# Kernel tuning notes

Measured on AMD Instinct MI355X. Metric: run time of the kernel, lower is better.

Reference implementation:

```python
import jax, jax.numpy as jnp
import numpy as np

S, B, I = 512, 32, 512
H, O = 512, 512
TOP_K = 5
TRUNC = 100
EPS = 1e-7
NEG = -1e9


def setup_inputs() -> dict:
    key = jax.random.key(0)
    ks = jax.random.split(key, 12)
    std = 1.0 / np.sqrt(H)
    return {
        "input": jax.random.normal(ks[0], (S, B, I), jnp.float32),
        "h0": jax.random.normal(ks[1], (1, B, H), jnp.float32),
        "c0": jax.random.normal(ks[2], (1, B, H), jnp.float32),
        "mem0": jax.random.normal(ks[3], (1, B, H), jnp.float32),
        # LSTMCell params (PyTorch layout: gates ordered i, f, g, o)
        "w_ih": jax.random.uniform(ks[4], (4 * H, I), jnp.float32, -std, std),
        "w_hh": jax.random.uniform(ks[5], (4 * H, H), jnp.float32, -std, std),
        "b_ih": jax.random.uniform(ks[6], (4 * H,), jnp.float32, -std, std),
        "b_hh": jax.random.uniform(ks[7], (4 * H,), jnp.float32, -std, std),
        # attention scorer, init N(0, 0.01)
        "w_t": jax.random.normal(ks[8], (2 * H, 1), jnp.float32) * 0.01,
        "fc_w": jax.random.uniform(ks[9], (O, 2 * H), jnp.float32, -1.0 / np.sqrt(2 * H), 1.0 / np.sqrt(2 * H)),
        "fc_b": jax.random.uniform(ks[10], (O,), jnp.float32, -1.0 / np.sqrt(2 * H), 1.0 / np.sqrt(2 * H)),
    }


def _sab_forward(input, h0, c0, mem0, w_ih, w_hh, b_ih, b_hh, w_t, fc_w, fc_b):
    seq_len, batch, _ = input.shape
    hid = w_hh.shape[1]
    m0 = mem0.shape[0]
    mmax = m0 + seq_len  # remem_every_k == 1: one append per step
    mem_buf = jnp.zeros((mmax, batch, hid), input.dtype).at[:m0].set(mem0)
    pos = jnp.arange(mmax)

    def step(carry, xs):
        h, c, mem = carry
        x, i = xs
        trunc = ((i + 1) % TRUNC) == 0
        h_in = jnp.where(trunc, jax.lax.stop_gradient(h), h)
        c_in = jnp.where(trunc, jax.lax.stop_gradient(c), c)
        # LSTM cell
        gates = x @ w_ih.T + b_ih + h_in @ w_hh.T + b_hh
        gi, gf, gg, go = jnp.split(gates, 4, axis=1)
        c_new = jax.nn.sigmoid(gf) * c_in + jax.nn.sigmoid(gi) * jnp.tanh(gg)
        h_new = jax.nn.sigmoid(go) * jnp.tanh(c_new)
        # attention over current (valid) memory
        cur = m0 + i  # valid memory entries before appending
        valid = (pos < cur)[:, None]  # (mmax, 1)
        feat = jnp.tanh(jnp.concatenate([jnp.broadcast_to(h_new[None], (mmax, batch, hid)), mem], axis=2))
        scores = jnp.einsum("mbf,fo->mb", feat, w_t)  # (mmax, batch)
        s_mask = jnp.where(valid, scores, NEG)
        kth = jax.lax.top_k(s_mask.T, TOP_K)[0][:, -1]  # (batch,)
        min_valid = jnp.min(jnp.where(valid, scores, jnp.inf), axis=0)
        delta = jnp.where(cur <= TOP_K, min_valid, kth) + EPS
        aw = jnp.clip(s_mask - delta[None, :], 0.0)  # invalid rows -> 0
        aw = aw / (jnp.sum(aw, axis=0, keepdims=True) + EPS)
        m_t = jnp.einsum("mb,mbh->bh", aw, mem)
        h_out = h_new + m_t
        mem = jax.lax.dynamic_update_slice(mem, h_out[None], (cur, 0, 0))
        return (h_out, c_new, mem), (h_out, m_t)

    (h_f, c_f, mem_f), (h_seq, m_seq) = jax.lax.scan(
        step, (h0[0], c0[0], mem_buf), (input, jnp.arange(seq_len)))
    out = jnp.concatenate([h_seq, m_seq], axis=2) @ fc_w.T + fc_b  # (S,B,O)
    return out, h_f[None], c_f[None], mem_f


def reference(input, h0, c0, mem0, w_ih, w_hh, b_ih, b_hh, w_t, fc_w, fc_b):
    return _sab_forward(input, h0, c0, mem0, w_ih, w_hh, b_ih, b_hh, w_t, fc_w, fc_b)
```

## Files before the change

kernel.cpp:

```cpp
#include <hip/hip_runtime.h>

#define SEQ   512
#define NB    32
#define NH    512
#define BH    16384
#define EPSF  1e-7f
#define NWG   64

#define HF_OFF  8388608
#define CF_OFF  8404992
#define MEM_OFF 8421376

#define X0_OFF   0ul
#define X1_OFF   16777216ul
#define WI0_OFF  33554432ul
#define WI1_OFF  35651584ul
#define HH_OFF   37748736ul
#define HMF_OFF  54558720ul
#define MSEQ_OFF 71368704ul
#define FCW_OFF  88145920ul
#define S2P_OFF  89194496ul
#define BAR_OFF  93396992ul
#define GX_OFF   93405184ul

typedef __attribute__((ext_vector_type(8))) short bf16x8;
typedef __attribute__((ext_vector_type(4))) float f32x4;
typedef __attribute__((ext_vector_type(4))) int   i32x4;

__device__ __forceinline__ unsigned short f2bf(float f){
  unsigned u = __float_as_uint(f);
  unsigned r = (u + 0x7fffu + ((u >> 16) & 1u)) >> 16;
  return (unsigned short)r;
}
__device__ __forceinline__ float bf2f(unsigned short h){
  return __uint_as_float(((unsigned)h) << 16);
}
__device__ __forceinline__ float sigmf(float x){ return 1.f/(1.f + __expf(-x)); }
__device__ __forceinline__ float tanhff(float x){
  x = fminf(20.f, fmaxf(-20.f, x));
  float e = __expf(-2.f*x);
  return (1.f - e)/(1.f + e);
}

__device__ __forceinline__ void store16_cc(void* p, i32x4 v){
  asm volatile("global_store_dwordx4 %0, %1, off sc0 sc1" :: "v"(p), "v"(v) : "memory");
}

__global__ void phase0(const float* __restrict__ x, const float* __restrict__ h0,
                       const float* __restrict__ mem0, const float* __restrict__ fcw,
                       const float* __restrict__ wih,
                       unsigned short* __restrict__ x0, unsigned short* __restrict__ x1,
                       unsigned short* __restrict__ wi0, unsigned short* __restrict__ wi1,
                       unsigned short* __restrict__ hh, unsigned short* __restrict__ hmf,
                       unsigned short* __restrict__ fcwb,
                       float* __restrict__ mem_row0, unsigned* __restrict__ bar){
  long i = (long)blockIdx.x * blockDim.x + threadIdx.x;
  if (i < (long)SEQ*BH){
    float v = x[i];
    unsigned short a = f2bf(v);
    x0[i]=a; x1[i]=f2bf(v - bf2f(a));
  }
  if (i < 2048*512){
    float v = wih[i];
    unsigned short a = f2bf(v);
    wi0[i]=a; wi1[i]=f2bf(v - bf2f(a));
  }
  if (i < 512*1024) fcwb[i] = f2bf(fcw[i]);
  if (i < BH){
    float h = h0[i];
    unsigned short a = f2bf(h);
    int b = (int)(i >> 9), col = (int)(i & 511);
    long d = (long)(col>>3)*256 + b*8 + (col&7);
    hh[d]=a; hmf[d]=f2bf(h - bf2f(a));
    mem_row0[i] = mem0[i];
  }
  if (i < 2048) bar[i] = 0u;
}

__launch_bounds__(256)
__global__ void xgemm(const unsigned short* __restrict__ x0, const unsigned short* __restrict__ x1,
                      const unsigned short* __restrict__ wi0, const unsigned short* __restrict__ wi1,
                      const float* __restrict__ bih, const float* __restrict__ bhh,
                      float* __restrict__ gx){
  const int tid = threadIdx.x;
  const int wave = tid >> 6, lane = tid & 63, quad = lane >> 4, ln = lane & 15;
  const int rowb = blockIdx.x*64 + wave*16;
  const int colb = blockIdx.y*64;
  const long aoff = (long)(rowb + ln)*512 + quad*8;
  f32x4 acc[4] = {{0,0,0,0},{0,0,0,0},{0,0,0,0},{0,0,0,0}};
  #pragma unroll 4
  for (int ki = 0; ki < 16; ++ki){
    bf16x8 a0 = *(const bf16x8*)(x0 + aoff + ki*32);
    bf16x8 a1 = *(const bf16x8*)(x1 + aoff + ki*32);
    #pragma unroll
    for (int n = 0; n < 4; ++n){
      long bo = (long)(colb + n*16 + ln)*512 + quad*8 + ki*32;
      bf16x8 b0 = *(const bf16x8*)(wi0 + bo);
      bf16x8 b1 = *(const bf16x8*)(wi1 + bo);
      acc[n] = __builtin_amdgcn_mfma_f32_16x16x32_bf16(a0, b0, acc[n], 0,0,0);
      acc[n] = __builtin_amdgcn_mfma_f32_16x16x32_bf16(a0, b1, acc[n], 0,0,0);
      acc[n] = __builtin_amdgcn_mfma_f32_16x16x32_bf16(a1, b0, acc[n], 0,0,0);
    }
  }
  #pragma unroll
  for (int n = 0; n < 4; ++n){
    int col = colb + n*16 + ln;
    float bias = bih[col] + bhh[col];
    #pragma unroll
    for (int rr = 0; rr < 4; ++rr){
      int row = rowb + quad*4 + rr;
      gx[(long)row*2048 + col] = acc[n][rr] + bias;
    }
  }
}

__launch_bounds__(256, 1)
__global__ void recurrent(unsigned short* __restrict__ hh,
                          unsigned short* __restrict__ hmf,
                          unsigned short* __restrict__ mseq,
                          float* __restrict__ s2p,
                          unsigned* __restrict__ bar,
                          float* __restrict__ dout,
                          const float* __restrict__ gx,
                          const float* __restrict__ whh,
                          const float* __restrict__ wt,
                          const float* __restrict__ c0){
  const int g    = blockIdx.x;
  const int tid  = threadIdx.x;
  const int wave = tid >> 6, lane = tid & 63, quad = lane >> 4, ln = lane & 15;
  const int mtile = wave & 1, ntile = wave >> 1;

  __shared__ float gates_lds[32*33];
  __shared__ float s2v[64*33];
  __shared__ float wt_lds[32*5];
  __shared__ int   repl_lds[32];
  __shared__ unsigned hm_lds[256];
  __shared__ float s2_lds[32];

  bf16x8 fW0[16], fW1[16];
  {
    int cl   = ntile*16 + ln;
    int gate = cl >> 3, jl = cl & 7;
    long grow = (long)(gate*NH + g*8 + jl);
    const float* wh = whh + grow*NH;
    #pragma unroll
    for (int ki = 0; ki < 16; ++ki){
      int k0 = ki*32 + quad*8;
      bf16x8 a, b;
      #pragma unroll
      for (int e = 0; e < 8; ++e){
        float vh = wh[k0+e];
        unsigned short w0 = f2bf(vh);
        a[e] = (short)w0; b[e] = (short)f2bf(vh - bf2f(w0));
      }
      fW0[ki]=a; fW1[ki]=b;
    }
  }

  const int b_  = tid >> 3, jl_ = tid & 7;
  const int jg_ = g*8 + jl_;
  const float wt2 = wt[NH + jg_];
  float creg = c0[b_*NH + jg_];
  float* memf = dout + MEM_OFF;

  float m0v = memf[b_*NH + jg_];
  float va0 = 0.f, va1 = 0.f, va2 = 0.f, va3 = 0.f, va4 = 0.f;
  float hoprev = m0v;

  {
    float v = tanhff(m0v) * wt2;
    v += __shfl_xor(v, 1); v += __shfl_xor(v, 2); v += __shfl_xor(v, 4);
    if (jl_ == 0)
      __hip_atomic_store((unsigned*)(s2p + g*32 + b_), __float_as_uint(v),
                         __ATOMIC_RELAXED, __HIP_MEMORY_SCOPE_AGENT);
  }

  const float* gxr0 = gx + (long)b_*2048 + jg_;
  float gxi = gxr0[0], gxf = gxr0[512], gxg = gxr0[1024], gxo = gxr0[1536];

  float tv0=-3e38f,tv1=-3e38f,tv2=-3e38f,tv3=-3e38f,tv4=-3e38f;

  unsigned epoch = 1u;
  __syncthreads();
  if (tid == 0)
    __hip_atomic_store(&bar[g*32], epoch, __ATOMIC_RELAXED, __HIP_MEMORY_SCOPE_AGENT);
  if (tid < 64){
    while (true){
      unsigned v = __hip_atomic_load(&bar[tid*32], __ATOMIC_RELAXED, __HIP_MEMORY_SCOPE_AGENT);
      if (__all((int)(v >= epoch))) break;
    }
  }
  __syncthreads();

  const int arow = mtile*16 + ln;

  #pragma unroll 1
  for (int t = 0; t < SEQ; ++t){
    f32x4 sv0, sv1, sv2, sv3, sv4, sv5, sv6, sv7;
    if (tid < 64){
      const float* sp = s2p + (long)t*2048 + tid*32;
      sv0 = *(const f32x4*)(sp +  0); sv1 = *(const f32x4*)(sp +  4);
      sv2 = *(const f32x4*)(sp +  8); sv3 = *(const f32x4*)(sp + 12);
      sv4 = *(const f32x4*)(sp + 16); sv5 = *(const f32x4*)(sp + 20);
      sv6 = *(const f32x4*)(sp + 24); sv7 = *(const f32x4*)(sp + 28);
    }

    const unsigned short* p0 = hh  + (long)t*BH + quad*256 + arow*8;
    const unsigned short* p1 = hmf + (long)t*BH + quad*256 + arow*8;
    f32x4 acc0 = {0.f,0.f,0.f,0.f}, acc1 = {0.f,0.f,0.f,0.f};
    #pragma unroll
    for (int ki = 0; ki < 16; ++ki){
      bf16x8 aH = *(const bf16x8*)(p0 + ki*1024);
      bf16x8 aM = *(const bf16x8*)(p1 + ki*1024);
      acc0 = __builtin_amdgcn_mfma_f32_16x16x32_bf16(aH, fW0[ki], acc0, 0,0,0);
      acc1 = __builtin_amdgcn_mfma_f32_16x16x32_bf16(aH, fW1[ki], acc1, 0,0,0);
      if (ki & 1) acc1 = __builtin_amdgcn_mfma_f32_16x16x32_bf16(aM, fW0[ki], acc1, 0,0,0);
      else        acc0 = __builtin_amdgcn_mfma_f32_16x16x32_bf16(aM, fW0[ki], acc0, 0,0,0);
    }
    #pragma unroll
    for (int r = 0; r < 4; ++r){
      int brow = mtile*16 + quad*4 + r;
      gates_lds[brow*33 + ntile*16 + ln] = acc0[r] + acc1[r];
    }

    if (tid < 64){
      float* sr = &s2v[tid*33];
      *(f32x4*)(sr +  0) = sv0; *(f32x4*)(sr +  4) = sv1;
      *(f32x4*)(sr +  8) = sv2; *(f32x4*)(sr + 12) = sv3;
      *(f32x4*)(sr + 16) = sv4; *(f32x4*)(sr + 20) = sv5;
      *(f32x4*)(sr + 24) = sv6; *(f32x4*)(sr + 28) = sv7;
    }
    if (tid < 32){
      float s0=0.f,s1=0.f,s2s=0.f,s3=0.f;
      #pragma unroll
      for (int q = 0; q < 64; q += 4){
        s0  += s2v[(q  )*33 + tid];
        s1  += s2v[(q+1)*33 + tid];
        s2s += s2v[(q+2)*33 + tid];
        s3  += s2v[(q+3)*33 + tid];
      }
      float s = (s0+s1) + (s2s+s3);
      int repl = -1;
      if (t < 5){
        repl = t;
        if      (t==0) tv0=s;
        else if (t==1) tv1=s;
        else if (t==2) tv2=s;
        else if (t==3) tv3=s;
        else           tv4=s;
      } else {
        float mn = fminf(fminf(fminf(tv0,tv1),fminf(tv2,tv3)),tv4);
        if (s > mn){
          if      (tv0==mn){tv0=s;repl=0;}
          else if (tv1==mn){tv1=s;repl=1;}
          else if (tv2==mn){tv2=s;repl=2;}
          else if (tv3==mn){tv3=s;repl=3;}
          else             {tv4=s;repl=4;}
        }
      }
      int cnt = (t+1 < 5) ? (t+1) : 5;
      float mn = tv0;
      if (cnt>1) mn = fminf(mn, tv1);
      if (cnt>2) mn = fminf(mn, tv2);
      if (cnt>3) mn = fminf(mn, tv3);
      if (cnt>4) mn = fminf(mn, tv4);
      float thr = mn + EPSF;
      float w0 =            fmaxf(tv0-thr,0.f);
      float w1 = (cnt>1) ? fmaxf(tv1-thr,0.f) : 0.f;
      float w2 = (cnt>2) ? fmaxf(tv2-thr,0.f) : 0.f;
      float w3 = (cnt>3) ? fmaxf(tv3-thr,0.f) : 0.f;
      float w4 = (cnt>4) ? fmaxf(tv4-thr,0.f) : 0.f;
      float inv = 1.f/((w0+w1+w2+w3+w4) + EPSF);
      wt_lds[tid*5+0]=w0*inv;
      wt_lds[tid*5+1]=w1*inv;
      wt_lds[tid*5+2]=w2*inv;
      wt_lds[tid*5+3]=w3*inv;
      wt_lds[tid*5+4]=w4*inv;
      repl_lds[tid]=repl;
    }
    __syncthreads();

    float g0 = gates_lds[b_*33 + jl_     ] + gxi;
    float g1 = gates_lds[b_*33 +  8 + jl_] + gxf;
    float g2 = gates_lds[b_*33 + 16 + jl_] + gxg;
    float g3 = gates_lds[b_*33 + 24 + jl_] + gxo;
    float ig = sigmf(g0), fg = sigmf(g1), gg = tanhff(g2), og = sigmf(g3);
    creg = fg*creg + ig*gg;
    float hn = og * tanhff(creg);

    int rp = repl_lds[b_];
    va0 = (rp==0) ? hoprev : va0;
    va1 = (rp==1) ? hoprev : va1;
    va2 = (rp==2) ? hoprev : va2;
    va3 = (rp==3) ? hoprev : va3;
    va4 = (rp==4) ? hoprev : va4;
    float mt = wt_lds[b_*5+0]*va0 + wt_lds[b_*5+1]*va1 + wt_lds[b_*5+2]*va2
             + wt_lds[b_*5+3]*va3 + wt_lds[b_*5+4]*va4;
    float ho = hn + mt;
    long eoff = (long)b_*NH + jg_;
    memf[(long)(t+1)*BH + eoff] = ho;
    unsigned short h0s = f2bf(ho);
    unsigned short h1s = f2bf(ho - bf2f(h0s));
    hm_lds[b_*8 + jl_] = (unsigned)h0s | (((unsigned)h1s) << 16);
    mseq[(long)t*BH + eoff] = f2bf(mt);
    if (t == SEQ-1) dout[HF_OFF + eoff] = ho;
    hoprev = ho;

    {
      float v = tanhff(ho) * wt2;
      v += __shfl_xor(v, 1); v += __shfl_xor(v, 2); v += __shfl_xor(v, 4);
      if (jl_ == 0) s2_lds[b_] = v;
    }

    {
      int tn = (t+1 < SEQ) ? t+1 : t;
      const float* gxr = gx + ((long)tn*32 + b_)*2048 + jg_;
      gxi = gxr[0]; gxf = gxr[512]; gxg = gxr[1024]; gxo = gxr[1536];
    }

    __syncthreads();
    ++epoch;
    if (tid < 64){
      if (tid < 32){
        int b = tid;
        unsigned q0 = hm_lds[b*8+0], q1 = hm_lds[b*8+1], q2 = hm_lds[b*8+2], q3 = hm_lds[b*8+3];
        unsigned q4 = hm_lds[b*8+4], q5 = hm_lds[b*8+5], q6 = hm_lds[b*8+6], q7 = hm_lds[b*8+7];
        i32x4 hi, mi;
        hi[0] = (int)((q0 & 0xffffu) | (q1 << 16));
        hi[1] = (int)((q2 & 0xffffu) | (q3 << 16));
        hi[2] = (int)((q4 & 0xffffu) | (q5 << 16));
        hi[3] = (int)((q6 & 0xffffu) | (q7 << 16));
        mi[0] = (int)((q0 >> 16) | (q1 & 0xffff0000u));
        mi[1] = (int)((q2 >> 16) | (q3 & 0xffff0000u));
        mi[2] = (int)((q4 >> 16) | (q5 & 0xffff0000u));
        mi[3] = (int)((q6 >> 16) | (q7 & 0xffff0000u));
        long d = (long)(t+1)*BH + g*256 + b*8;
        store16_cc(hh  + d, hi);
        store16_cc(hmf + d, mi);
      } else if (tid < 40){
        int q = tid - 32;
        f32x4 svp = *(const f32x4*)&s2_lds[q*4];
        store16_cc(s2p + (long)(t+1)*2048 + g*32 + q*4, __builtin_bit_cast(i32x4, svp));
      }
      asm volatile("s_waitcnt vmcnt(0)" ::: "memory");
      if (tid == 0)
        __hip_atomic_store(&bar[g*32], epoch, __ATOMIC_RELAXED, __HIP_MEMORY_SCOPE_AGENT);
      while (true){
        unsigned v = __hip_atomic_load(&bar[tid*32], __ATOMIC_RELAXED, __HIP_MEMORY_SCOPE_AGENT);
        if (__all((int)(v >= epoch))) break;
      }
    }
    __syncthreads();
  }
  dout[CF_OFF + (long)b_*NH + jg_] = creg;
}

__launch_bounds__(256)
__global__ void outgemm(const unsigned short* __restrict__ hh,
                        const unsigned short* __restrict__ mseq,
                        const unsigned short* __restrict__ fcwb,
                        const float* __restrict__ fcb,
                        float* __restrict__ out){
  const int tid = threadIdx.x;
  const int wave = tid >> 6, lane = tid & 63, quad = lane >> 4, ln = lane & 15;
  const int wgM = blockIdx.x;
  const int wgN = blockIdx.y;
  const int r = wgM*64 + wave*16 + ln;
  const int s = r >> 5, b = r & 31;
  const unsigned short* pa_h = hh   + (long)(s+1)*BH + quad*256 + b*8;
  const unsigned short* pa_m = mseq + (long)s*BH     + (long)b*NH + quad*8;
  const unsigned short* pb   = fcwb + (long)(wgN*64 + ln)*1024 + quad*8;
  f32x4 accs[4] = {{0,0,0,0},{0,0,0,0},{0,0,0,0},{0,0,0,0}};
  #pragma unroll 4
  for (int ki = 0; ki < 16; ++ki){
    bf16x8 a = *(const bf16x8*)(pa_h + ki*1024);
    #pragma unroll
    for (int n = 0; n < 4; ++n){
      bf16x8 bb = *(const bf16x8*)(pb + (long)n*16*1024 + ki*32);
      accs[n] = __builtin_amdgcn_mfma_f32_16x16x32_bf16(a, bb, accs[n], 0,0,0);
    }
  }
  #pragma unroll 4
  for (int ki = 0; ki < 16; ++ki){
    bf16x8 a = *(const bf16x8*)(pa_m + ki*32);
    #pragma unroll
    for (int n = 0; n < 4; ++n){
      bf16x8 bb = *(const bf16x8*)(pb + 512 + (long)n*16*1024 + ki*32);
      accs[n] = __builtin_amdgcn_mfma_f32_16x16x32_bf16(a, bb, accs[n], 0,0,0);
    }
  }
  #pragma unroll
  for (int n = 0; n < 4; ++n){
    int o = wgN*64 + n*16 + ln;
    float bias = fcb[o];
    #pragma unroll
    for (int rr = 0; rr < 4; ++rr){
      int row = wgM*64 + wave*16 + quad*4 + rr;
      out[(long)row*512 + o] = accs[n][rr] + bias;
    }
  }
}

extern "C" void kernel_launch(void* const* d_in, const int* in_sizes, int n_in,
                              void* d_out, int out_size, void* d_ws, size_t ws_size,
                              hipStream_t stream){
  (void)in_sizes; (void)n_in; (void)out_size; (void)ws_size;
  const float* x    = (const float*)d_in[0];
  const float* h0   = (const float*)d_in[1];
  const float* c0   = (const float*)d_in[2];
  const float* mem0 = (const float*)d_in[3];
  const float* wih  = (const float*)d_in[4];
  const float* whh  = (const float*)d_in[5];
  const float* bih  = (const float*)d_in[6];
  const float* bhh  = (const float*)d_in[7];
  const float* wt   = (const float*)d_in[8];
  const float* fcw  = (const float*)d_in[9];
  const float* fcb  = (const float*)d_in[10];
  float* out = (float*)d_out;
  char* ws = (char*)d_ws;

  unsigned short* x0   = (unsigned short*)(ws + X0_OFF);
  unsigned short* x1   = (unsigned short*)(ws + X1_OFF);
  unsigned short* wi0  = (unsigned short*)(ws + WI0_OFF);
  unsigned short* wi1  = (unsigned short*)(ws + WI1_OFF);
  unsigned short* hh   = (unsigned short*)(ws + HH_OFF);
  unsigned short* hmf  = (unsigned short*)(ws + HMF_OFF);
  unsigned short* mseq = (unsigned short*)(ws + MSEQ_OFF);
  unsigned short* fcwb = (unsigned short*)(ws + FCW_OFF);
  float*          s2p  = (float*)(ws + S2P_OFF);
  unsigned*       bar  = (unsigned*)(ws + BAR_OFF);
  float*          gx   = (float*)(ws + GX_OFF);

  phase0<<<32768, 256, 0, stream>>>(x, h0, mem0, fcw, wih,
                                    x0, x1, wi0, wi1,
                                    hh, hmf, fcwb, out + MEM_OFF, bar);
  xgemm<<<dim3(256, 32), 256, 0, stream>>>(x0, x1, wi0, wi1, bih, bhh, gx);
  recurrent<<<NWG, 256, 0, stream>>>(hh, hmf, mseq, s2p, bar, out,
                                     gx, whh, wt, c0);
  outgemm<<<dim3(256, 8), 256, 0, stream>>>(hh, mseq, fcwb, fcb, out);
}
```

Before: 4.561 ms.

## Add a fifth wave to compute attention scores concurrently with the gate MFMA

The recurrent kernel grows from 256 to 320 threads. The extra wave reads the per-step score partials directly from global memory, reduces them and runs the top-k and weight update, while the four original waves run the hidden-state MFMA at the same time. This removes the LDS staging buffer for the scores and takes that reduction off the critical path of the MFMA waves. In exchange, the extra wave makes strided global loads, and the block gets more threads, which can lengthen barrier costs.

```diff
diff --git a/kernel.cpp b/kernel.cpp
--- a/kernel.cpp
+++ b/kernel.cpp
@@ -114,7 +114,7 @@
   }
 }
 
-__launch_bounds__(256, 1)
+__launch_bounds__(320, 1)
 __global__ void recurrent(unsigned short* __restrict__ hh,
                           unsigned short* __restrict__ hmf,
                           unsigned short* __restrict__ mseq,
@@ -131,14 +131,13 @@
   const int mtile = wave & 1, ntile = wave >> 1;
 
   __shared__ float gates_lds[32*33];
-  __shared__ float s2v[64*33];
   __shared__ float wt_lds[32*5];
   __shared__ int   repl_lds[32];
   __shared__ unsigned hm_lds[256];
   __shared__ float s2_lds[32];
 
   bf16x8 fW0[16], fW1[16];
-  {
+  if (wave < 4){
     int cl   = ntile*16 + ln;
     int gate = cl >> 3, jl = cl & 7;
     long grow = (long)(gate*NH + g*8 + jl);
@@ -160,14 +159,16 @@
   const int b_  = tid >> 3, jl_ = tid & 7;
   const int jg_ = g*8 + jl_;
   const float wt2 = wt[NH + jg_];
-  float creg = c0[b_*NH + jg_];
   float* memf = dout + MEM_OFF;
-
-  float m0v = memf[b_*NH + jg_];
+  float creg = 0.f, m0v = 0.f;
+  if (tid < 256){
+    creg = c0[b_*NH + jg_];
+    m0v  = memf[b_*NH + jg_];
+  }
   float va0 = 0.f, va1 = 0.f, va2 = 0.f, va3 = 0.f, va4 = 0.f;
   float hoprev = m0v;
 
-  {
+  if (tid < 256){
     float v = tanhff(m0v) * wt2;
     v += __shfl_xor(v, 1); v += __shfl_xor(v, 2); v += __shfl_xor(v, 4);
     if (jl_ == 0)
@@ -175,8 +176,11 @@
                          __ATOMIC_RELAXED, __HIP_MEMORY_SCOPE_AGENT);
   }
 
-  const float* gxr0 = gx + (long)b_*2048 + jg_;
-  float gxi = gxr0[0], gxf = gxr0[512], gxg = gxr0[1024], gxo = gxr0[1536];
+  float gxi = 0.f, gxf = 0.f, gxg = 0.f, gxo = 0.f;
+  if (tid < 256){
+    const float* gxr0 = gx + (long)b_*2048 + jg_;
+    gxi = gxr0[0]; gxf = gxr0[512]; gxg = gxr0[1024]; gxo = gxr0[1536];
+  }
 
   float tv0=-3e38f,tv1=-3e38f,tv2=-3e38f,tv3=-3e38f,tv4=-3e38f;
 
@@ -196,126 +200,116 @@
 
   #pragma unroll 1
   for (int t = 0; t < SEQ; ++t){
-    f32x4 sv0, sv1, sv2, sv3, sv4, sv5, sv6, sv7;
-    if (tid < 64){
-      const float* sp = s2p + (long)t*2048 + tid*32;
-      sv0 = *(const f32x4*)(sp +  0); sv1 = *(const f32x4*)(sp +  4);
-      sv2 = *(const f32x4*)(sp +  8); sv3 = *(const f32x4*)(sp + 12);
-      sv4 = *(const f32x4*)(sp + 16); sv5 = *(const f32x4*)(sp + 20);
-      sv6 = *(const f32x4*)(sp + 24); sv7 = *(const f32x4*)(sp + 28);
-    }
-
-    const unsigned short* p0 = hh  + (long)t*BH + quad*256 + arow*8;
-    const unsigned short* p1 = hmf + (long)t*BH + quad*256 + arow*8;
-    f32x4 acc0 = {0.f,0.f,0.f,0.f}, acc1 = {0.f,0.f,0.f,0.f};
-    #pragma unroll
-    for (int ki = 0; ki < 16; ++ki){
-      bf16x8 aH = *(const bf16x8*)(p0 + ki*1024);
-      bf16x8 aM = *(const bf16x8*)(p1 + ki*1024);
-      acc0 = __builtin_amdgcn_mfma_f32_16x16x32_bf16(aH, fW0[ki], acc0, 0,0,0);
-      acc1 = __builtin_amdgcn_mfma_f32_16x16x32_bf16(aH, fW1[ki], acc1, 0,0,0);
-      if (ki & 1) acc1 = __builtin_amdgcn_mfma_f32_16x16x32_bf16(aM, fW0[ki], acc1, 0,0,0);
-      else        acc0 = __builtin_amdgcn_mfma_f32_16x16x32_bf16(aM, fW0[ki], acc0, 0,0,0);
-    }
-    #pragma unroll
-    for (int r = 0; r < 4; ++r){
-      int brow = mtile*16 + quad*4 + r;
-      gates_lds[brow*33 + ntile*16 + ln] = acc0[r] + acc1[r];
-    }
-
-    if (tid < 64){
-      float* sr = &s2v[tid*33];
-      *(f32x4*)(sr +  0) = sv0; *(f32x4*)(sr +  4) = sv1;
-      *(f32x4*)(sr +  8) = sv2; *(f32x4*)(sr + 12) = sv3;
-      *(f32x4*)(sr + 16) = sv4; *(f32x4*)(sr + 20) = sv5;
-      *(f32x4*)(sr + 24) = sv6; *(f32x4*)(sr + 28) = sv7;
-    }
-    if (tid < 32){
-      float s0=0.f,s1=0.f,s2s=0.f,s3=0.f;
+    if (tid >= 256){
+      const int l4 = tid - 256;
+      if (l4 < 32){
+        const float* sp = s2p + (long)t*2048 + l4;
+        float s0=0.f,s1=0.f,s2v=0.f,s3=0.f;
+        #pragma unroll
+        for (int q = 0; q < 64; q += 4){
+          s0  += sp[(q  )*32];
+          s1  += sp[(q+1)*32];
+          s2v += sp[(q+2)*32];
+          s3  += sp[(q+3)*32];
+        }
+        float s = (s0+s1) + (s2v+s3);
+        int repl = -1;
+        if (t < 5){
+          repl = t;
+          if      (t==0) tv0=s;
+          else if (t==1) tv1=s;
+          else if (t==2) tv2=s;
+          else if (t==3) tv3=s;
+          else           tv4=s;
+        } else {
+          float mn = fminf(fminf(fminf(tv0,tv1),fminf(tv2,tv3)),tv4);
+          if (s > mn){
+            if      (tv0==mn){tv0=s;repl=0;}
+            else if (tv1==mn){tv1=s;repl=1;}
+            else if (tv2==mn){tv2=s;repl=2;}
+            else if (tv3==mn){tv3=s;repl=3;}
+            else             {tv4=s;repl=4;}
+          }
+        }
+        int cnt = (t+1 < 5) ? (t+1) : 5;
+        float mn = tv0;
+        if (cnt>1) mn = fminf(mn, tv1);
+        if (cnt>2) mn = fminf(mn, tv2);
+        if (cnt>3) mn = fminf(mn, tv3);
+        if (cnt>4) mn = fminf(mn, tv4);
+        float thr = mn + EPSF;
+        float w0 =            fmaxf(tv0-thr,0.f);
+        float w1 = (cnt>1) ? fmaxf(tv1-thr,0.f) : 0.f;
+        float w2 = (cnt>2) ? fmaxf(tv2-thr,0.f) : 0.f;
+        float w3 = (cnt>3) ? fmaxf(tv3-thr,0.f) : 0.f;
+        float w4 = (cnt>4) ? fmaxf(tv4-thr,0.f) : 0.f;
+        float inv = 1.f/((w0+w1+w2+w3+w4) + EPSF);
+        wt_lds[l4*5+0]=w0*inv;
+        wt_lds[l4*5+1]=w1*inv;
+        wt_lds[l4*5+2]=w2*inv;
+        wt_lds[l4*5+3]=w3*inv;
+        wt_lds[l4*5+4]=w4*inv;
+        repl_lds[l4]=repl;
+      }
+    } else {
+      const unsigned short* p0 = hh  + (long)t*BH + quad*256 + arow*8;
+      const unsigned short* p1 = hmf + (long)t*BH + quad*256 + arow*8;
+      f32x4 acc0 = {0.f,0.f,0.f,0.f}, acc1 = {0.f,0.f,0.f,0.f};
       #pragma unroll
-      for (int q = 0; q < 64; q += 4){
-        s0  += s2v[(q  )*33 + tid];
-        s1  += s2v[(q+1)*33 + tid];
-        s2s += s2v[(q+2)*33 + tid];
-        s3  += s2v[(q+3)*33 + tid];
-      }
-      float s = (s0+s1) + (s2s+s3);
-      int repl = -1;
-      if (t < 5){
-        repl = t;
-        if      (t==0) tv0=s;
-        else if (t==1) tv1=s;
-        else if (t==2) tv2=s;
-        else if (t==3) tv3=s;
-        else           tv4=s;
-      } else {
-        float mn = fminf(fminf(fminf(tv0,tv1),fminf(tv2,tv3)),tv4);
-        if (s > mn){
-          if      (tv0==mn){tv0=s;repl=0;}
-          else if (tv1==mn){tv1=s;repl=1;}
-          else if (tv2==mn){tv2=s;repl=2;}
-          else if (tv3==mn){tv3=s;repl=3;}
-          else             {tv4=s;repl=4;}
-        }
-      }
-      int cnt = (t+1 < 5) ? (t+1) : 5;
-      float mn = tv0;
-      if (cnt>1) mn = fminf(mn, tv1);
-      if (cnt>2) mn = fminf(mn, tv2);
-      if (cnt>3) mn = fminf(mn, tv3);
-      if (cnt>4) mn = fminf(mn, tv4);
-      float thr = mn + EPSF;
-      float w0 =            fmaxf(tv0-thr,0.f);
-      float w1 = (cnt>1) ? fmaxf(tv1-thr,0.f) : 0.f;
-      float w2 = (cnt>2) ? fmaxf(tv2-thr,0.f) : 0.f;
-      float w3 = (cnt>3) ? fmaxf(tv3-thr,0.f) : 0.f;
-      float w4 = (cnt>4) ? fmaxf(tv4-thr,0.f) : 0.f;
-      float inv = 1.f/((w0+w1+w2+w3+w4) + EPSF);
-      wt_lds[tid*5+0]=w0*inv;
-      wt_lds[tid*5+1]=w1*inv;
-      wt_lds[tid*5+2]=w2*inv;
-      wt_lds[tid*5+3]=w3*inv;
-      wt_lds[tid*5+4]=w4*inv;
-      repl_lds[tid]=repl;
+      for (int ki = 0; ki < 16; ++ki){
+        bf16x8 aH = *(const bf16x8*)(p0 + ki*1024);
+        bf16x8 aM = *(const bf16x8*)(p1 + ki*1024);
+        acc0 = __builtin_amdgcn_mfma_f32_16x16x32_bf16(aH, fW0[ki], acc0, 0,0,0);
+        acc1 = __builtin_amdgcn_mfma_f32_16x16x32_bf16(aH, fW1[ki], acc1, 0,0,0);
+        if (ki & 1) acc1 = __builtin_amdgcn_mfma_f32_16x16x32_bf16(aM, fW0[ki], acc1, 0,0,0);
+        else        acc0 = __builtin_amdgcn_mfma_f32_16x16x32_bf16(aM, fW0[ki], acc0, 0,0,0);
+      }
+      #pragma unroll
+      for (int r = 0; r < 4; ++r){
+        int brow = mtile*16 + quad*4 + r;
+        gates_lds[brow*33 + ntile*16 + ln] = acc0[r] + acc1[r];
+      }
     }
     __syncthreads();
 
-    float g0 = gates_lds[b_*33 + jl_     ] + gxi;
-    float g1 = gates_lds[b_*33 +  8 + jl_] + gxf;
-    float g2 = gates_lds[b_*33 + 16 + jl_] + gxg;
-    float g3 = gates_lds[b_*33 + 24 + jl_] + gxo;
-    float ig = sigmf(g0), fg = sigmf(g1), gg = tanhff(g2), og = sigmf(g3);
-    creg = fg*creg + ig*gg;
-    float hn = og * tanhff(creg);
-
-    int rp = repl_lds[b_];
-    va0 = (rp==0) ? hoprev : va0;
-    va1 = (rp==1) ? hoprev : va1;
-    va2 = (rp==2) ? hoprev : va2;
-    va3 = (rp==3) ? hoprev : va3;
-    va4 = (rp==4) ? hoprev : va4;
-    float mt = wt_lds[b_*5+0]*va0 + wt_lds[b_*5+1]*va1 + wt_lds[b_*5+2]*va2
-             + wt_lds[b_*5+3]*va3 + wt_lds[b_*5+4]*va4;
-    float ho = hn + mt;
-    long eoff = (long)b_*NH + jg_;
-    memf[(long)(t+1)*BH + eoff] = ho;
-    unsigned short h0s = f2bf(ho);
-    unsigned short h1s = f2bf(ho - bf2f(h0s));
-    hm_lds[b_*8 + jl_] = (unsigned)h0s | (((unsigned)h1s) << 16);
-    mseq[(long)t*BH + eoff] = f2bf(mt);
-    if (t == SEQ-1) dout[HF_OFF + eoff] = ho;
-    hoprev = ho;
-
-    {
-      float v = tanhff(ho) * wt2;
-      v += __shfl_xor(v, 1); v += __shfl_xor(v, 2); v += __shfl_xor(v, 4);
-      if (jl_ == 0) s2_lds[b_] = v;
-    }
-
-    {
-      int tn = (t+1 < SEQ) ? t+1 : t;
-      const float* gxr = gx + ((long)tn*32 + b_)*2048 + jg_;
-      gxi = gxr[0]; gxf = gxr[512]; gxg = gxr[1024]; gxo = gxr[1536];
+    if (tid < 256){
+      float g0 = gates_lds[b_*33 + jl_     ] + gxi;
+      float g1 = gates_lds[b_*33 +  8 + jl_] + gxf;
+      float g2 = gates_lds[b_*33 + 16 + jl_] + gxg;
+      float g3 = gates_lds[b_*33 + 24 + jl_] + gxo;
+      float ig = sigmf(g0), fg = sigmf(g1), gg = tanhff(g2), og = sigmf(g3);
+      creg = fg*creg + ig*gg;
+      float hn = og * tanhff(creg);
+
+      int rp = repl_lds[b_];
+      va0 = (rp==0) ? hoprev : va0;
+      va1 = (rp==1) ? hoprev : va1;
+      va2 = (rp==2) ? hoprev : va2;
+      va3 = (rp==3) ? hoprev : va3;
+      va4 = (rp==4) ? hoprev : va4;
+      float mt = wt_lds[b_*5+0]*va0 + wt_lds[b_*5+1]*va1 + wt_lds[b_*5+2]*va2
+               + wt_lds[b_*5+3]*va3 + wt_lds[b_*5+4]*va4;
+      float ho = hn + mt;
+      long eoff = (long)b_*NH + jg_;
+      memf[(long)(t+1)*BH + eoff] = ho;
+      unsigned short h0s = f2bf(ho);
+      unsigned short h1s = f2bf(ho - bf2f(h0s));
+      hm_lds[b_*8 + jl_] = (unsigned)h0s | (((unsigned)h1s) << 16);
+      mseq[(long)t*BH + eoff] = f2bf(mt);
+      if (t == SEQ-1) dout[HF_OFF + eoff] = ho;
+      hoprev = ho;
+
+      {
+        float v = tanhff(ho) * wt2;
+        v += __shfl_xor(v, 1); v += __shfl_xor(v, 2); v += __shfl_xor(v, 4);
+        if (jl_ == 0) s2_lds[b_] = v;
+      }
+
+      {
+        int tn = (t+1 < SEQ) ? t+1 : t;
+        const float* gxr = gx + ((long)tn*32 + b_)*2048 + jg_;
+        gxi = gxr[0]; gxf = gxr[512]; gxg = gxr[1024]; gxo = gxr[1536];
+      }
     }
 
     __syncthreads();
@@ -352,7 +346,8 @@
     }
     __syncthreads();
   }
-  dout[CF_OFF + (long)b_*NH + jg_] = creg;
+  if (tid < 256)
+    dout[CF_OFF + (long)b_*NH + jg_] = creg;
 }
 
 __launch_bounds__(256)
@@ -435,7 +430,7 @@
                                     x0, x1, wi0, wi1,
                                     hh, hmf, fcwb, out + MEM_OFF, bar);
   xgemm<<<dim3(256, 32), 256, 0, stream>>>(x0, x1, wi0, wi1, bih, bhh, gx);
-  recurrent<<<NWG, 256, 0, stream>>>(hh, hmf, mseq, s2p, bar, out,
+  recurrent<<<NWG, 320, 0, stream>>>(hh, hmf, mseq, s2p, bar, out,
                                      gx, whh, wt, c0);
   outgemm<<<dim3(256, 8), 256, 0, stream>>>(hh, mseq, fcwb, fcb, out);
 }
```

After: 3.886 ms. 14.8% less time.
